# Kernel tuning notes

Measured on AMD Instinct MI355X. Metric: run time of the kernel, lower is better.

## Reference

```python
import jax, jax.numpy as jnp
import numpy as np
from jax import lax

B = 8          # batch
IMG = 224      # image size
PATCH = 16     # patch size / stride
D = 384        # embed_dim = d_model = d_inner (expand=1)
DEPTH = 24     # number of blocks
N = 16         # d_state
K = 4          # d_conv
R = 24         # dt_rank = ceil(D/16)
H = D * 4 * 2 // 3   # SwiGLU hidden = 1024
L = (IMG // PATCH) ** 2  # 196 tokens


def setup_inputs() -> dict:
    ks = iter(jax.random.split(jax.random.key(0), 40))
    def rn(shape, s=0.02):
        return jax.random.normal(next(ks), shape, jnp.float32) * s
    inp = {}
    inp["x"] = jax.random.normal(next(ks), (B, 3, IMG, IMG), jnp.float32)
    inp["patch_w"] = rn((D, 3, PATCH, PATCH))
    inp["patch_b"] = jnp.zeros((D,), jnp.float32)
    inp["norm1_w"] = jnp.ones((DEPTH, D), jnp.float32)
    inp["norm1_b"] = jnp.zeros((DEPTH, D), jnp.float32)
    inp["in_proj_w"] = rn((DEPTH, 2 * D, D))
    inp["conv_w"] = rn((DEPTH, D, K), 0.1)
    inp["conv_b"] = jnp.zeros((DEPTH, D), jnp.float32)
    inp["x_proj_w"] = rn((DEPTH, R + 2 * N, D))
    inp["dt_proj_w"] = rn((DEPTH, D, R), 0.1)
    inp["dt_proj_b"] = rn((DEPTH, D), 0.1)
    # S4D-real init: A = -exp(A_log), A_log = log(1..N)
    inp["A_log"] = jnp.tile(jnp.log(jnp.arange(1, N + 1, dtype=jnp.float32))[None, None, :], (DEPTH, D, 1))
    inp["D_skip"] = jnp.ones((DEPTH, D), jnp.float32)
    inp["out_proj_w"] = rn((DEPTH, D, D))
    inp["norm2_w"] = jnp.ones((DEPTH, D), jnp.float32)
    inp["norm2_b"] = jnp.zeros((DEPTH, D), jnp.float32)
    inp["w1_w"] = rn((DEPTH, H, D)); inp["w1_b"] = jnp.zeros((DEPTH, H), jnp.float32)
    inp["w2_w"] = rn((DEPTH, H, D)); inp["w2_b"] = jnp.zeros((DEPTH, H), jnp.float32)
    inp["w3_w"] = rn((DEPTH, D, H)); inp["w3_b"] = jnp.zeros((DEPTH, D), jnp.float32)
    inp["normf_w"] = jnp.ones((D,), jnp.float32)
    inp["normf_b"] = jnp.zeros((D,), jnp.float32)
    return inp


def _ln(x, w, b, eps=1e-5):
    m = x.mean(-1, keepdims=True)
    v = jnp.mean((x - m) ** 2, axis=-1, keepdims=True)
    return (x - m) / jnp.sqrt(v + eps) * w + b


def _mamba(x, in_w, cw, cb, xp_w, dtw, dtb, a_log, d_skip, ow):
    # x: [B, L, D]; Mamba with expand=1, bimamba 'none'
    bsz, seq, _ = x.shape
    xz = jnp.einsum('bld,ed->ble', x, in_w)        # [B, L, 2D]
    xc, z = jnp.split(xz, 2, axis=-1)
    # causal depthwise conv1d, kernel K, padding K-1, truncated to L
    xpd = jnp.pad(xc, ((0, 0), (K - 1, 0), (0, 0)))
    xconv = sum(xpd[:, k:k + seq, :] * cw[:, k] for k in range(K)) + cb
    xa = jax.nn.silu(xconv)
    dbc = jnp.einsum('bld,ed->ble', xa, xp_w)      # [B, L, R+2N]
    dt = jax.nn.softplus(jnp.einsum('blr,dr->bld', dbc[..., :R], dtw) + dtb)  # [B, L, D]
    Bm = dbc[..., R:R + N]                         # [B, L, N]
    Cm = dbc[..., R + N:]                          # [B, L, N]
    A = -jnp.exp(a_log)                            # [D, N]

    def step(h, t):
        dt_t, B_t, C_t, x_t = t                    # [B,D],[B,N],[B,N],[B,D]
        h = h * jnp.exp(dt_t[..., None] * A) + (dt_t * x_t)[..., None] * B_t[:, None, :]
        return h, jnp.einsum('bdn,bn->bd', h, C_t)

    h0 = jnp.zeros((bsz, D, N), x.dtype)
    _, ys = lax.scan(step, h0, (dt.transpose(1, 0, 2), Bm.transpose(1, 0, 2),
                                Cm.transpose(1, 0, 2), xa.transpose(1, 0, 2)))
    y = ys.transpose(1, 0, 2) + d_skip * xa
    y = y * jax.nn.silu(z)
    return jnp.einsum('bld,ed->ble', y, ow)


def _forward(x, patch_w, patch_b, norm1_w, norm1_b, in_proj_w, conv_w, conv_b,
             x_proj_w, dt_proj_w, dt_proj_b, A_log, D_skip, out_proj_w,
             norm2_w, norm2_b, w1_w, w1_b, w2_w, w2_b, w3_w, w3_b, normf_w, normf_b):
    p = lax.conv_general_dilated(x, patch_w, (PATCH, PATCH), 'VALID',
                                 dimension_numbers=('NCHW', 'OIHW', 'NCHW'))
    p = p + patch_b[None, :, None, None]
    h = p.reshape(p.shape[0], D, -1).transpose(0, 2, 1)   # [B, L, D]
    for i in range(DEPTH):
        h = h + _mamba(_ln(h, norm1_w[i], norm1_b[i]), in_proj_w[i], conv_w[i], conv_b[i],
                       x_proj_w[i], dt_proj_w[i], dt_proj_b[i], A_log[i], D_skip[i], out_proj_w[i])
        hn = _ln(h, norm2_w[i], norm2_b[i])
        hid = jax.nn.silu(hn @ w1_w[i].T + w1_b[i]) * (hn @ w2_w[i].T + w2_b[i])
        h = h + hid @ w3_w[i].T + w3_b[i]
    return _ln(h, normf_w, normf_b)


def reference(x, patch_w, patch_b, norm1_w, norm1_b, in_proj_w, conv_w, conv_b,
              x_proj_w, dt_proj_w, dt_proj_b, A_log, D_skip, out_proj_w,
              norm2_w, norm2_b, w1_w, w1_b, w2_w, w2_b, w3_w, w3_b, normf_w, normf_b):
    return _forward(x, patch_w, patch_b, norm1_w, norm1_b, in_proj_w, conv_w, conv_b,
                    x_proj_w, dt_proj_w, dt_proj_b, A_log, D_skip, out_proj_w,
                    norm2_w, norm2_b, w1_w, w1_b, w2_w, w2_b, w3_w, w3_b, normf_w, normf_b)
```

## Files before the change

kernel.cpp:

```cpp
#include <hip/hip_runtime.h>
#include <math.h>

#define BB 8
#define LL 196
#define DD 384
#define NDEPTH 24
#define NST 16
#define RRANK 24
#define HHID 1024
#define MROWS (BB*LL)
#define NCH 28
#define CHL 7

typedef float f32x4 __attribute__((ext_vector_type(4)));
typedef short s16x8 __attribute__((ext_vector_type(8)));
typedef short s16x4 __attribute__((ext_vector_type(4)));
typedef __bf16 b16x8 __attribute__((ext_vector_type(8)));
typedef unsigned short u16;
typedef unsigned int u32;

#if defined(__has_builtin)
#  if __has_builtin(__builtin_amdgcn_global_load_lds)
#    define HAS_GLL 1
#  endif
#endif
#ifndef HAS_GLL
#  define HAS_GLL 0
#endif

__device__ __forceinline__ float sigmoidf_(float x){ return 1.f/(1.f+__expf(-x)); }

__device__ __forceinline__ u16 f2bf(float f){
    u32 u = __builtin_bit_cast(u32, f);
    u32 r = (u + 0x7fffu + ((u >> 16) & 1u)) >> 16;
    return (u16)r;
}
__device__ __forceinline__ float bf2f(u16 v){
    u32 u = ((u32)v) << 16;
    return __builtin_bit_cast(float, u);
}

__device__ __forceinline__ void gll16(const u16* g, void* lds){
#if HAS_GLL
    __builtin_amdgcn_global_load_lds(
        (const __attribute__((address_space(1))) unsigned int*)g,
        (__attribute__((address_space(3))) unsigned int*)lds, 16, 0, 0);
#endif
}

template<int N> __device__ __forceinline__ void waitbar(){
    if constexpr (N==0) asm volatile("s_waitcnt vmcnt(0) lgkmcnt(0)\ns_barrier" ::: "memory");
    else if constexpr (N==4) asm volatile("s_waitcnt vmcnt(4) lgkmcnt(0)\ns_barrier" ::: "memory");
    else if constexpr (N==8) asm volatile("s_waitcnt vmcnt(8) lgkmcnt(0)\ns_barrier" ::: "memory");
    else asm volatile("s_waitcnt vmcnt(0) lgkmcnt(0)\ns_barrier" ::: "memory");
    __builtin_amdgcn_sched_barrier(0);
}
__device__ __forceinline__ void bar_release(){
    asm volatile("s_waitcnt lgkmcnt(0)\ns_barrier" ::: "memory");
    __builtin_amdgcn_sched_barrier(0);
}

template<typename V>
__device__ __forceinline__ auto mfma_try(V a, V b, f32x4 c, int)
    -> decltype(__builtin_amdgcn_mfma_f32_16x16x32_bf16(a, b, c, 0, 0, 0))
{ return __builtin_amdgcn_mfma_f32_16x16x32_bf16(a, b, c, 0, 0, 0); }

template<typename V>
__device__ __forceinline__ f32x4 mfma_try(V a, V b, f32x4 c, long)
{
    return __builtin_amdgcn_mfma_f32_16x16x32_bf16(
        __builtin_bit_cast(b16x8, a), __builtin_bit_cast(b16x8, b), c, 0, 0, 0);
}
__device__ __forceinline__ f32x4 mfma_bf16(s16x8 a, s16x8 b, f32x4 c){ return mfma_try(a, b, c, 0); }

__global__ __launch_bounds__(64) void ln_k(const float* __restrict__ X,
    const float* __restrict__ w, const float* __restrict__ b, float* __restrict__ Y)
{
    int row = blockIdx.x;
    int lane = threadIdx.x;
    const float* x = X + (size_t)row*DD;
    float v[6]; float s=0.f, s2=0.f;
    #pragma unroll
    for (int j=0;j<6;j++){ float t = x[lane + j*64]; v[j]=t; s+=t; s2+=t*t; }
    #pragma unroll
    for (int o=32;o>=1;o>>=1){ s += __shfl_xor(s,o); s2 += __shfl_xor(s2,o); }
    float m = s*(1.f/DD);
    float var = s2*(1.f/DD) - m*m;
    float rstd = rsqrtf(var + 1e-5f);
    #pragma unroll
    for (int j=0;j<6;j++){
        int c = lane + j*64;
        Y[(size_t)row*DD + c] = (v[j]-m)*rstd*w[c] + b[c];
    }
}

__global__ void gather_k(const float* __restrict__ x, u16* __restrict__ P)
{
    int idx = blockIdx.x*blockDim.x + threadIdx.x;
    if (idx >= MROWS*768) return;
    int k = idx % 768;
    int bl = idx / 768;
    int l = bl % LL;
    int b = bl / LL;
    int c = k >> 8;
    int rem = k & 255;
    int dy = rem >> 4, dx = rem & 15;
    int py = l / 14, px = l % 14;
    P[idx] = f2bf(x[(((size_t)b*3 + c)*224 + (py*16+dy))*224 + (px*16+dx)]);
}

__device__ __forceinline__ int swz(int row, int chunk){
    return (row << 7) + ((chunk ^ (row & 7)) << 4);
}

template<int EPI, bool WB, int CFG, int PRO, int K>
__global__ __launch_bounds__(256) void mgemm_k(
    const u16* __restrict__ A, const float* __restrict__ Af,
    const float* __restrict__ lnw, const float* __restrict__ lnb,
    const void* __restrict__ W1v, const void* __restrict__ W2v,
    const float* __restrict__ bias1, const float* __restrict__ bias2,
    float* __restrict__ Cf, u16* __restrict__ Cb,
    int M, int N)
{
    constexpr int  BM   = (CFG==1)?32:16;
    constexpr int  FM   = (CFG==2)?1:2;
    constexpr int  FN   = 2;
    constexpr int  NAR  = (BM+31)/32;
    constexpr bool DUAL = (EPI==4);
    constexpr int  ABY  = BM*128;
    constexpr int  BBY  = 128*128;
    constexpr bool ASY  = WB && (HAS_GLL==1);
    constexpr int  NKT  = K >> 6;
    constexpr int  NLW  = DUAL ? 8 : 4;
    __shared__ __attribute__((aligned(16))) char sm[2*ABY + 2*BBY + (DUAL ? 2*BBY : 0)];
    char* A0 = sm;          char* A1 = sm + ABY;
    char* B0 = sm + 2*ABY;  char* B1 = B0 + BBY;
    char* C0 = B1 + BBY;    char* C1 = C0 + BBY;

    const int tid = threadIdx.x;
    const int row0 = blockIdx.y * BM;
    const int col0 = blockIdx.x << 7;
    const int w = tid >> 6, lane = tid & 63;
    const int wn  = w;
    const int lr = lane & 15, lk = lane >> 4;
    const int ar0 = tid >> 3, ac8 = tid & 7;
    const bool apart = (CFG != 2) || (tid < 128);

    const u16*   W1b = (const u16*)W1v;
    const u16*   W2b = (const u16*)W2v;
    const float* W1f = (const float*)W1v;
    const float* W2f = (const float*)W2v;

    f32x4 acc [FM][FN] = {};
    f32x4 acc2[FM][FN] = {};

    s16x8 aval[NAR];
    s16x8 bval[4], b2val[4];
    float4 bvf[8], b2vf[8];
    s16x8 lnr[(PRO==1)?NKT:1];

    if (PRO == 1 && apart){
        const float* xrow = Af + (size_t)(row0 + ar0)*DD;
        float4 va[6], vb[6];
        float s = 0.f, s2 = 0.f;
        #pragma unroll
        for (int j=0;j<6;j++){
            va[j] = *(const float4*)(xrow + j*64 + ac8*8);
            vb[j] = *(const float4*)(xrow + j*64 + ac8*8 + 4);
            s  += va[j].x+va[j].y+va[j].z+va[j].w + vb[j].x+vb[j].y+vb[j].z+vb[j].w;
            s2 += va[j].x*va[j].x+va[j].y*va[j].y+va[j].z*va[j].z+va[j].w*va[j].w
                + vb[j].x*vb[j].x+vb[j].y*vb[j].y+vb[j].z*vb[j].z+vb[j].w*vb[j].w;
        }
        #pragma unroll
        for (int o=1;o<8;o<<=1){ s += __shfl_xor(s,o); s2 += __shfl_xor(s2,o); }
        float m = s*(1.f/DD);
        float rstd = rsqrtf(s2*(1.f/DD) - m*m + 1e-5f);
        #pragma unroll
        for (int j=0;j<6;j++){
            int c0 = j*64 + ac8*8;
            float4 w0 = *(const float4*)(lnw + c0);
            float4 w1 = *(const float4*)(lnw + c0 + 4);
            float4 b0 = *(const float4*)(lnb + c0);
            float4 b1 = *(const float4*)(lnb + c0 + 4);
            s16x8 ov;
            ov[0]=(short)f2bf((va[j].x-m)*rstd*w0.x+b0.x);
            ov[1]=(short)f2bf((va[j].y-m)*rstd*w0.y+b0.y);
            ov[2]=(short)f2bf((va[j].z-m)*rstd*w0.z+b0.z);
            ov[3]=(short)f2bf((va[j].w-m)*rstd*w0.w+b0.w);
            ov[4]=(short)f2bf((vb[j].x-m)*rstd*w1.x+b1.x);
            ov[5]=(short)f2bf((vb[j].y-m)*rstd*w1.y+b1.y);
            ov[6]=(short)f2bf((vb[j].z-m)*rstd*w1.z+b1.z);
            ov[7]=(short)f2bf((vb[j].w-m)*rstd*w1.w+b1.w);
            if (j < NKT) lnr[j] = ov;
        }
    }

    auto stageAsync = [&](int kt, char* bA, char* bB, char* bC){
        const int lhi = lane >> 3, llo = lane & 7;
        const int colel = (kt << 6) + ((llo ^ lhi) << 3);
        if (PRO == 0){
            constexpr int ACH = BM/8;
            #pragma unroll
            for (int ci = w; ci < ACH; ci += 4){
                int gr = row0 + ci*8 + lhi;
                gll16(A + (size_t)gr*K + colel, bA + ci*1024);
            }
        }
        #pragma unroll
        for (int i=0;i<4;i++){
            int ci = w*4 + i;
            int gb = col0 + ci*8 + lhi;
            gll16(W1b + (size_t)gb*K + colel, bB + ci*1024);
        }
        if (DUAL){
            #pragma unroll
            for (int i=0;i<4;i++){
                int ci = w*4 + i;
                int gb = col0 + ci*8 + lhi;
                gll16(W2b + (size_t)gb*K + colel, bC + ci*1024);
            }
        }
    };

    auto loadT = [&](int kt){
        const int kb = kt << 6;
        if (PRO == 0 && apart){
            #pragma unroll
            for (int i=0;i<NAR;i++){
                int gr = row0 + i*32 + ar0;
                if (gr < M) aval[i] = *(const s16x8*)(A + (size_t)gr*K + kb + ac8*8);
                else        aval[i] = s16x8{0,0,0,0,0,0,0,0};
            }
        }
        if (WB){
            #pragma unroll
            for (int i=0;i<4;i++){
                int gb = col0 + i*32 + ar0;
                if (gb < N) bval[i] = *(const s16x8*)(W1b + (size_t)gb*K + kb + ac8*8);
                else        bval[i] = s16x8{0,0,0,0,0,0,0,0};
            }
            if (DUAL){
                #pragma unroll
                for (int i=0;i<4;i++){
                    int gb = col0 + i*32 + ar0;
                    if (gb < N) b2val[i] = *(const s16x8*)(W2b + (size_t)gb*K + kb + ac8*8);
                    else        b2val[i] = s16x8{0,0,0,0,0,0,0,0};
                }
            }
        } else {
            #pragma unroll
            for (int i=0;i<8;i++){
                int ss = i*256 + tid;
                int r = ss >> 4, q = ss & 15;
                int gb = col0 + r;
                if (gb < N) bvf[i] = *(const float4*)(W1f + (size_t)gb*K + kb + q*4);
                else        bvf[i] = float4{0,0,0,0};
            }
            if (DUAL){
                #pragma unroll
                for (int i=0;i<8;i++){
                    int ss = i*256 + tid;
                    int r = ss >> 4, q = ss & 15;
                    int gb = col0 + r;
                    if (gb < N) b2vf[i] = *(const float4*)(W2f + (size_t)gb*K + kb + q*4);
                    else        b2vf[i] = float4{0,0,0,0};
                }
            }
        }
    };
    auto writeT = [&](char* bA, char* bB, char* bC){
        if (PRO == 0 && apart){
            #pragma unroll
            for (int i=0;i<NAR;i++)
                *(s16x8*)(bA + swz(i*32 + ar0, ac8)) = aval[i];
        }
        if (WB){
            #pragma unroll
            for (int i=0;i<4;i++)
                *(s16x8*)(bB + swz(i*32 + ar0, ac8)) = bval[i];
            if (DUAL){
                #pragma unroll
                for (int i=0;i<4;i++)
                    *(s16x8*)(bC + swz(i*32 + ar0, ac8)) = b2val[i];
            }
        } else {
            #pragma unroll
            for (int i=0;i<8;i++){
                int ss = i*256 + tid;
                int r = ss >> 4, q = ss & 15;
                float4 v = bvf[i];
                s16x4 cv = { (short)f2bf(v.x), (short)f2bf(v.y), (short)f2bf(v.z), (short)f2bf(v.w) };
                int off = (r << 7) + (((q >> 1) ^ (r & 7)) << 4) + ((q & 1) << 3);
                *(s16x4*)(bB + off) = cv;
            }
            if (DUAL){
                #pragma unroll
                for (int i=0;i<8;i++){
                    int ss = i*256 + tid;
                    int r = ss >> 4, q = ss & 15;
                    float4 v = b2vf[i];
                    s16x4 cv = { (short)f2bf(v.x), (short)f2bf(v.y), (short)f2bf(v.z), (short)f2bf(v.w) };
                    int off = (r << 7) + (((q >> 1) ^ (r & 7)) << 4) + ((q & 1) << 3);
                    *(s16x4*)(bC + off) = cv;
                }
            }
        }
    };

    auto compute = [&](char* cA, char* cB, char* cC){
        #pragma unroll
        for (int ks=0; ks<2; ks++){
            s16x8 af[FM], bfr[FN];
            #pragma unroll
            for (int m=0;m<FM;m++)
                af[m] = *(const s16x8*)(cA + swz(m*16 + lr, ks*4 + lk));
            #pragma unroll
            for (int n=0;n<FN;n++)
                bfr[n] = *(const s16x8*)(cB + swz(wn*32 + n*16 + lr, ks*4 + lk));
            #pragma unroll
            for (int m=0;m<FM;m++)
                #pragma unroll
                for (int n=0;n<FN;n++)
                    acc[m][n] = mfma_bf16(af[m], bfr[n], acc[m][n]);
            if (DUAL){
                s16x8 b2r[FN];
                #pragma unroll
                for (int n=0;n<FN;n++)
                    b2r[n] = *(const s16x8*)(cC + swz(wn*32 + n*16 + lr, ks*4 + lk));
                #pragma unroll
                for (int m=0;m<FM;m++)
                    #pragma unroll
                    for (int n=0;n<FN;n++)
                        acc2[m][n] = mfma_bf16(af[m], b2r[n], acc2[m][n]);
            }
        }
    };

    if (ASY){
        stageAsync(0, A0, B0, C0);
        if (NKT > 1) stageAsync(1, A1, B1, C1);
        if (PRO == 1 && apart){
            *(s16x8*)(A0 + swz(ar0, ac8)) = lnr[0];
            if (NKT > 1) *(s16x8*)(A1 + swz(ar0, ac8)) = lnr[(1 < NKT) ? 1 : 0];
        }
        if (NKT > 1) waitbar<NLW>(); else waitbar<0>();
        #pragma unroll
        for (int kt=0; kt<NKT; kt++){
            if (kt & 1) compute(A1, B1, C1);
            else        compute(A0, B0, C0);
            if (kt+1 < NKT){
                bar_release();
                if (kt+2 < NKT){
                    char* rA = (kt&1)?A1:A0; char* rB = (kt&1)?B1:B0; char* rC = (kt&1)?C1:C0;
                    stageAsync(kt+2, rA, rB, rC);
                    if (PRO == 1 && apart)
                        *(s16x8*)(rA + swz(ar0, ac8)) = lnr[(kt+2 < NKT) ? (kt+2) : 0];
                    waitbar<NLW>();
                } else {
                    waitbar<0>();
                }
            }
        }
    } else {
        loadT(0); writeT(A0, B0, C0);
        if (PRO == 1 && apart) *(s16x8*)(A0 + swz(ar0, ac8)) = lnr[0];
        __syncthreads();
        #pragma unroll
        for (int kt=0; kt<NKT; kt++){
            const bool more = (kt+1 < NKT);
            char* nA = (kt&1)?A0:A1; char* nB = (kt&1)?B0:B1; char* nC = (kt&1)?C0:C1;
            if (more){
                loadT(kt+1);
                if (PRO == 1 && apart) *(s16x8*)(nA + swz(ar0, ac8)) = lnr[(kt+1 < NKT) ? (kt+1) : 0];
            }
            if (kt & 1) compute(A1, B1, C1);
            else        compute(A0, B0, C0);
            if (more) writeT(nA, nB, nC);
            __syncthreads();
        }
    }

    #pragma unroll
    for (int n=0;n<FN;n++){
        int gc = col0 + wn*32 + n*16 + lr;
        if (gc >= N) continue;
        float b1 = 0.f, b2 = 0.f;
        if (EPI==1||EPI==3||EPI==4) b1 = bias1[gc];
        if (EPI==4) b2 = bias2[gc];
        #pragma unroll
        for (int m=0;m<FM;m++){
            #pragma unroll
            for (int r=0;r<4;r++){
                int gr = row0 + m*16 + lk*4 + r;
                if (gr >= M) continue;
                float v = acc[m][n][r];
                if (EPI==1||EPI==3) v += b1;
                if (EPI==2||EPI==3) v += Cf[(size_t)gr*N + gc];
                if (EPI==4){
                    float v1 = v + b1;
                    float v2 = acc2[m][n][r] + b2;
                    Cb[(size_t)gr*N + gc] = f2bf(v1 * sigmoidf_(v1) * v2);
                } else if (EPI==6){
                    Cb[(size_t)gr*N + gc] = f2bf(v);
                } else {
                    Cf[(size_t)gr*N + gc] = v;
                }
            }
        }
    }
}

template<int K>
__device__ __forceinline__ int off_a(int row, int chunk){
    return row*(K*2) + ((chunk ^ (row & 7)) << 4);
}

template<bool WB>
__global__ __launch_bounds__(256) void xproj_k(
    const u16* __restrict__ xzb,
    const float* __restrict__ cw, const float* __restrict__ cb,
    const void* __restrict__ Wv,
    float* __restrict__ dbc)
{
    constexpr int K = DD, N = 56;
    constexpr int ABY = 16*K*2;
    __shared__ __attribute__((aligned(16))) char sm[ABY + 2*16384];
    char* sA = sm;
    char* B0 = sm + ABY;
    char* B1 = B0 + 16384;

    const int tid = threadIdx.x;
    const int row0 = blockIdx.x * 16;
    const int wv = tid >> 6, lane = tid & 63;
    const int lr = lane & 15, lk = lane >> 4;
    const int ar0 = tid >> 3, ac8 = tid & 7;

    const u16*   Wb = (const u16*)Wv;
    const float* Wf = (const float*)Wv;

    f32x4 acc[2] = {};
    s16x8 bval[4];
    float4 bvf[8];

    auto loadB = [&](int kt){
        const int kb = kt << 6;
        if (WB){
            #pragma unroll
            for (int i=0;i<4;i++){
                int gb = i*32 + ar0;
                if (gb < N) bval[i] = *(const s16x8*)(Wb + (size_t)gb*K + kb + ac8*8);
                else        bval[i] = s16x8{0,0,0,0,0,0,0,0};
            }
        } else {
            #pragma unroll
            for (int i=0;i<8;i++){
                int ss = i*256 + tid;
                int r = ss >> 4, q = ss & 15;
                if (r < N) bvf[i] = *(const float4*)(Wf + (size_t)r*K + kb + q*4);
                else       bvf[i] = float4{0,0,0,0};
            }
        }
    };
    auto writeB = [&](char* bB){
        if (WB){
            #pragma unroll
            for (int i=0;i<4;i++)
                *(s16x8*)(bB + swz(i*32 + ar0, ac8)) = bval[i];
        } else {
            #pragma unroll
            for (int i=0;i<8;i++){
                int ss = i*256 + tid;
                int r = ss >> 4, q = ss & 15;
                float4 v = bvf[i];
                s16x4 cv = { (short)f2bf(v.x), (short)f2bf(v.y), (short)f2bf(v.z), (short)f2bf(v.w) };
                int off = (r << 7) + (((q >> 1) ^ (r & 7)) << 4) + ((q & 1) << 3);
                *(s16x4*)(bB + off) = cv;
            }
        }
    };

    loadB(0);

    #pragma unroll
    for (int r=0;r<4;r++){
        int rl = wv*4 + r, gr = row0 + rl;
        if (lane < 48){
            int l = gr % LL, bb = gr / LL;
            int d0 = lane*8;
            float a[8];
            #pragma unroll
            for (int j=0;j<8;j++) a[j] = cb[d0+j];
            #pragma unroll
            for (int t=0;t<4;t++){
                int ls = l - 3 + t;
                if (ls >= 0){
                    s16x8 xv = *(const s16x8*)(xzb + (size_t)(bb*LL+ls)*768 + d0);
                    #pragma unroll
                    for (int j=0;j<8;j++)
                        a[j] = fmaf(bf2f((u16)xv[j]), cw[(d0+j)*4+t], a[j]);
                }
            }
            s16x8 ov;
            #pragma unroll
            for (int j=0;j<8;j++)
                ov[j] = (short)f2bf(a[j]*sigmoidf_(a[j]));
            *(s16x8*)(sA + off_a<K>(rl, lane)) = ov;
        }
    }

    writeB(B0);
    __syncthreads();

    constexpr int nkt = K >> 6;
    #pragma unroll
    for (int kt=0; kt<nkt; kt++){
        const bool more = (kt+1 < nkt);
        if (more) loadB(kt+1);
        char* cB = (kt & 1) ? B1 : B0;
        #pragma unroll
        for (int ks=0; ks<2; ks++){
            s16x8 af = *(const s16x8*)(sA + off_a<K>(lr, kt*8 + ks*4 + lk));
            #pragma unroll
            for (int n=0;n<2;n++){
                s16x8 bfr = *(const s16x8*)(cB + swz(wv*32 + n*16 + lr, ks*4 + lk));
                acc[n] = mfma_bf16(af, bfr, acc[n]);
            }
        }
        if (more) writeB((kt & 1) ? B0 : B1);
        __syncthreads();
    }

    #pragma unroll
    for (int n=0;n<2;n++){
        int gc = wv*32 + n*16 + lr;
        if (gc >= N) continue;
        #pragma unroll
        for (int r=0;r<4;r++){
            int gr = row0 + lk*4 + r;
            dbc[(size_t)gr*N + gc] = acc[n][r];
        }
    }
}

__global__ void cvtw_k(const float* __restrict__ s, u16* __restrict__ d, int n)
{
    int i = blockIdx.x*blockDim.x + threadIdx.x;
    int idx = i*4;
    if (idx + 4 <= n){
        float4 v = *(const float4*)(s + idx);
        s16x4 cv = { (short)f2bf(v.x), (short)f2bf(v.y), (short)f2bf(v.z), (short)f2bf(v.w) };
        *(s16x4*)(d + idx) = cv;
    } else {
        for (int j=idx;j<n;j++) d[j] = f2bf(s[j]);
    }
}

__global__ __launch_bounds__(384) void scanA_k(
    const float* __restrict__ dbc, const u16* __restrict__ xzb,
    const float* __restrict__ cw, const float* __restrict__ cb,
    const float* __restrict__ dtw, const float* __restrict__ dtb,
    const float* __restrict__ a_log,
    float* __restrict__ Pout, float* __restrict__ Sout,
    float2* __restrict__ dtxv)
{
    int b = blockIdx.x / NCH;
    int c = blockIdx.x % NCH;
    int d = threadIdx.x;
    __shared__ float Ds[CHL][56];
    for (int t = threadIdx.x; t < CHL*56; t += 384){
        int j = t/56, q = t%56;
        Ds[j][q] = dbc[(size_t)(b*LL + c*CHL + j)*56 + q];
    }
    __syncthreads();
    float cwr[4];
    #pragma unroll
    for (int k=0;k<4;k++) cwr[k] = cw[d*4+k];
    float cbv = cb[d];
    float dtwr[RRANK];
    #pragma unroll
    for (int r=0;r<RRANK;r++) dtwr[r] = dtw[d*RRANK + r];
    float dtbv = dtb[d];
    float Aa[NST];
    #pragma unroll
    for (int n=0;n<NST;n++) Aa[n] = -__expf(a_log[d*NST+n]);
    int l0 = c*CHL;
    float p3=0.f, p2=0.f, p1=0.f;
    if (l0 >= 3) p3 = bf2f(xzb[(size_t)(b*LL+l0-3)*768 + d]);
    if (l0 >= 2) p2 = bf2f(xzb[(size_t)(b*LL+l0-2)*768 + d]);
    if (l0 >= 1) p1 = bf2f(xzb[(size_t)(b*LL+l0-1)*768 + d]);
    float hst[NST], P[NST];
    #pragma unroll
    for (int n=0;n<NST;n++){ hst[n]=0.f; P[n]=1.f; }
    #pragma unroll
    for (int j=0;j<CHL;j++){
        int row = b*LL + l0 + j;
        float cur = bf2f(xzb[(size_t)row*768 + d]);
        float a = cbv;
        a = fmaf(p3, cwr[0], a); a = fmaf(p2, cwr[1], a);
        a = fmaf(p1, cwr[2], a); a = fmaf(cur, cwr[3], a);
        p3 = p2; p2 = p1; p1 = cur;
        float xv = a * sigmoidf_(a);
        float t = dtbv;
        #pragma unroll
        for (int r=0;r<RRANK;r++) t = fmaf(dtwr[r], Ds[j][r], t);
        float dtv = (t > 20.f) ? t : log1pf(__expf(t));
        dtxv[(size_t)row*DD + d] = float2{dtv, xv};
        float du = dtv*xv;
        #pragma unroll
        for (int n=0;n<NST;n++){
            float e = __expf(dtv*Aa[n]);
            hst[n] = fmaf(hst[n], e, du*Ds[j][24+n]);
            P[n] *= e;
        }
    }
    size_t base = ((size_t)(b*NCH + c)*DD + d)*NST;
    #pragma unroll
    for (int n=0;n<NST;n++){ Pout[base+n]=P[n]; Sout[base+n]=hst[n]; }
}

__global__ __launch_bounds__(384) void scanC_k(
    const float* __restrict__ dbc, const float2* __restrict__ dtxv,
    const u16* __restrict__ xzb, const float* __restrict__ a_log,
    const float* __restrict__ Pin, const float* __restrict__ Sin,
    const float* __restrict__ dskip,
    u16* __restrict__ yg)
{
    int b = blockIdx.x / NCH;
    int c = blockIdx.x % NCH;
    int d = threadIdx.x;
    __shared__ float Ds[CHL][56];
    for (int t = threadIdx.x; t < CHL*56; t += 384){
        int j = t/56, q = t%56;
        Ds[j][q] = dbc[(size_t)(b*LL + c*CHL + j)*56 + q];
    }
    __syncthreads();
    float hst[NST];
    #pragma unroll
    for (int n=0;n<NST;n++) hst[n]=0.f;
    for (int cc=0; cc<c; cc++){
        size_t base = ((size_t)(b*NCH + cc)*DD + d)*NST;
        #pragma unroll
        for (int n=0;n<NST;n++)
            hst[n] = fmaf(Pin[base+n], hst[n], Sin[base+n]);
    }
    float Aa[NST];
    #pragma unroll
    for (int n=0;n<NST;n++) Aa[n] = -__expf(a_log[d*NST+n]);
    float dsk = dskip[d];
    int l0 = c*CHL;
    #pragma unroll
    for (int j=0;j<CHL;j++){
        int row = b*LL + l0 + j;
        float2 dx = dtxv[(size_t)row*DD + d];
        float dtv = dx.x, xv = dx.y;
        float du = dtv*xv;
        float y = 0.f;
        #pragma unroll
        for (int n=0;n<NST;n++){
            float e = __expf(dtv*Aa[n]);
            hst[n] = fmaf(hst[n], e, du*Ds[j][24+n]);
            y = fmaf(hst[n], Ds[j][40+n], y);
        }
        float zv = bf2f(xzb[(size_t)row*768 + 384 + d]);
        float g = zv * sigmoidf_(zv);
        yg[(size_t)row*DD + d] = f2bf((y + dsk*xv)*g);
    }
}

template<int EPI, int CFG, int PRO, int K>
static void mg(bool wb, dim3 g, hipStream_t s,
               const void* A, const float* Af, const float* lnw, const float* lnb,
               const void* Wb, const void* Wf, const void* W2b, const void* W2f,
               const float* b1, const float* b2, float* Cf, u16* Cb,
               int M, int N)
{
    if (wb) mgemm_k<EPI,true ,CFG,PRO,K><<<g,256,0,s>>>((const u16*)A, Af, lnw, lnb, Wb, W2b, b1, b2, Cf, Cb, M, N);
    else    mgemm_k<EPI,false,CFG,PRO,K><<<g,256,0,s>>>((const u16*)A, Af, lnw, lnb, Wf, W2f, b1, b2, Cf, Cb, M, N);
}

extern "C" void kernel_launch(void* const* d_in, const int* in_sizes, int n_in,
                              void* d_out, int out_size, void* d_ws, size_t ws_size,
                              hipStream_t stream)
{
    const float* x         = (const float*)d_in[0];
    const float* patch_w   = (const float*)d_in[1];
    const float* patch_b   = (const float*)d_in[2];
    const float* norm1_w   = (const float*)d_in[3];
    const float* norm1_b   = (const float*)d_in[4];
    const float* in_proj_w = (const float*)d_in[5];
    const float* conv_w    = (const float*)d_in[6];
    const float* conv_b    = (const float*)d_in[7];
    const float* x_proj_w  = (const float*)d_in[8];
    const float* dt_w      = (const float*)d_in[9];
    const float* dt_b      = (const float*)d_in[10];
    const float* A_log     = (const float*)d_in[11];
    const float* D_skip    = (const float*)d_in[12];
    const float* out_w     = (const float*)d_in[13];
    const float* norm2_w   = (const float*)d_in[14];
    const float* norm2_b   = (const float*)d_in[15];
    const float* w1_w      = (const float*)d_in[16];
    const float* w1_b      = (const float*)d_in[17];
    const float* w2_w      = (const float*)d_in[18];
    const float* w2_b      = (const float*)d_in[19];
    const float* w3_w      = (const float*)d_in[20];
    const float* w3_b      = (const float*)d_in[21];
    const float* normf_w   = (const float*)d_in[22];
    const float* normf_b   = (const float*)d_in[23];

    char* wsb = (char*)d_ws;
    size_t o = 0;
    auto take = [&](size_t bytes) -> char* {
        char* p = wsb + o;
        o += (bytes + 255) & ~(size_t)255;
        return p;
    };

    float* h    = (float*)take((size_t)602112*4);
    float* dbc  = (float*)take((size_t)87808*4);
    float* Pb   = (float*)take((size_t)BB*NCH*DD*NST*4);
    float* Sb   = (float*)take((size_t)BB*NCH*DD*NST*4);
    float2* dtxv= (float2*)take((size_t)MROWS*DD*8);
    u16*  xzb   = (u16*)take((size_t)1204224*2);
    u16*  yg    = (u16*)take((size_t)602112*2);
    u16*  hid   = (u16*)take((size_t)1605632*2);
    u16*  patches = hid;

    const size_t NPW = 294912, NIN = 7077888, NOUT = 3538944,
                 NW1 = 9437184, NW2 = 9437184, NW3 = 9437184, NXP = 516096;
    u16* wcP = (u16*)take(NPW*2);
    u16* wcI = (u16*)take(NIN*2);
    u16* wcO = (u16*)take(NOUT*2);
    u16* wc1 = (u16*)take(NW1*2);
    u16* wc2 = (u16*)take(NW2*2);
    u16* wc3 = (u16*)take(NW3*2);
    u16* wcX = (u16*)take(NXP*2);
    bool wb = (ws_size >= o);

    if (wb){
        cvtw_k<<<(int)((NPW/4+255)/256), 256, 0, stream>>>(patch_w, wcP, (int)NPW);
        cvtw_k<<<(int)((NIN/4+255)/256), 256, 0, stream>>>(in_proj_w, wcI, (int)NIN);
        cvtw_k<<<(int)((NOUT/4+255)/256),256, 0, stream>>>(out_w, wcO, (int)NOUT);
        cvtw_k<<<(int)((NW1/4+255)/256), 256, 0, stream>>>(w1_w, wc1, (int)NW1);
        cvtw_k<<<(int)((NW2/4+255)/256), 256, 0, stream>>>(w2_w, wc2, (int)NW2);
        cvtw_k<<<(int)((NW3/4+255)/256), 256, 0, stream>>>(w3_w, wc3, (int)NW3);
        cvtw_k<<<(int)((NXP/4+255)/256), 256, 0, stream>>>(x_proj_w, wcX, (int)NXP);
    }

    const int GY32 = MROWS/32;
    const int GY16 = MROWS/16;

    gather_k<<<(MROWS*768+255)/256, 256, 0, stream>>>(x, patches);
    mg<1,2,0,768>(wb, dim3(3,GY16), stream, patches, nullptr, nullptr, nullptr,
              wcP, patch_w, nullptr, nullptr, patch_b, nullptr, h, nullptr, MROWS, DD);

    for (int i=0;i<NDEPTH;i++){
        mg<6,1,1,384>(wb, dim3(6,GY32), stream, nullptr, h, norm1_w + i*DD, norm1_b + i*DD,
                  wcI + (size_t)i*768*DD, in_proj_w + (size_t)i*768*DD, nullptr, nullptr,
                  nullptr, nullptr, nullptr, xzb, MROWS, 768);
        if (wb) xproj_k<true ><<<GY16, 256, 0, stream>>>(xzb, conv_w + i*DD*4, conv_b + i*DD,
                                                         wcX + (size_t)i*56*DD, dbc);
        else    xproj_k<false><<<GY16, 256, 0, stream>>>(xzb, conv_w + i*DD*4, conv_b + i*DD,
                                                         x_proj_w + (size_t)i*56*DD, dbc);
        scanA_k<<<BB*NCH, 384, 0, stream>>>(dbc, xzb, conv_w + i*DD*4, conv_b + i*DD,
                                            dt_w + (size_t)i*DD*RRANK, dt_b + i*DD,
                                            A_log + (size_t)i*DD*NST, Pb, Sb, dtxv);
        scanC_k<<<BB*NCH, 384, 0, stream>>>(dbc, dtxv, xzb, A_log + (size_t)i*DD*NST,
                                            Pb, Sb, D_skip + i*DD, yg);
        mg<2,2,0,384>(wb, dim3(3,GY16), stream, yg, nullptr, nullptr, nullptr,
                  wcO + (size_t)i*DD*DD, out_w + (size_t)i*DD*DD, nullptr, nullptr,
                  nullptr, nullptr, h, nullptr, MROWS, DD);
        mg<4,1,1,384>(wb, dim3(8,GY32), stream, nullptr, h, norm2_w + i*DD, norm2_b + i*DD,
                  wc1 + (size_t)i*HHID*DD, w1_w + (size_t)i*HHID*DD,
                  wc2 + (size_t)i*HHID*DD, w2_w + (size_t)i*HHID*DD,
                  w1_b + i*HHID, w2_b + i*HHID, nullptr, hid, MROWS, HHID);
        mg<3,2,0,1024>(wb, dim3(3,GY16), stream, hid, nullptr, nullptr, nullptr,
                  wc3 + (size_t)i*DD*HHID, w3_w + (size_t)i*DD*HHID, nullptr, nullptr,
                  w3_b + i*DD, nullptr, h, nullptr, MROWS, DD);
    }

    ln_k<<<MROWS, 64, 0, stream>>>(h, normf_w, normf_b, (float*)d_out);
}
```

Measured before the change: 2.408 ms.

## Fuse chunked scan passes into one kernel with per-batch spin barrier

Merges the two selective-scan kernels into a single launch. Each block keeps its dt and x values in registers and waits on a per-batch atomic counter until every chunk of that batch has written its carry (P, S), then runs the second pass directly. This removes one launch per layer and the dtxv round trip through global memory. In exchange it depends on all 224 blocks being co-resident to avoid deadlock, and adds spin-wait and fence overhead.

```diff
diff --git a/kernel.cpp b/kernel.cpp
--- a/kernel.cpp
+++ b/kernel.cpp
@@ -555,13 +555,18 @@
     }
 }
 
-__global__ __launch_bounds__(384) void scanA_k(
+__global__ void zflag_k(u32* __restrict__ f){
+    if (threadIdx.x < NDEPTH*BB) f[threadIdx.x] = 0u;
+}
+
+__global__ __launch_bounds__(384) void scanAC_k(
     const float* __restrict__ dbc, const u16* __restrict__ xzb,
     const float* __restrict__ cw, const float* __restrict__ cb,
     const float* __restrict__ dtw, const float* __restrict__ dtb,
     const float* __restrict__ a_log,
     float* __restrict__ Pout, float* __restrict__ Sout,
-    float2* __restrict__ dtxv)
+    const float* __restrict__ dskip, u16* __restrict__ yg,
+    u32* __restrict__ flag)
 {
     int b = blockIdx.x / NCH;
     int c = blockIdx.x % NCH;
@@ -572,6 +577,7 @@
         Ds[j][q] = dbc[(size_t)(b*LL + c*CHL + j)*56 + q];
     }
     __syncthreads();
+
     float cwr[4];
     #pragma unroll
     for (int k=0;k<4;k++) cwr[k] = cw[d*4+k];
@@ -583,87 +589,79 @@
     float Aa[NST];
     #pragma unroll
     for (int n=0;n<NST;n++) Aa[n] = -__expf(a_log[d*NST+n]);
+
     int l0 = c*CHL;
     float p3=0.f, p2=0.f, p1=0.f;
     if (l0 >= 3) p3 = bf2f(xzb[(size_t)(b*LL+l0-3)*768 + d]);
     if (l0 >= 2) p2 = bf2f(xzb[(size_t)(b*LL+l0-2)*768 + d]);
     if (l0 >= 1) p1 = bf2f(xzb[(size_t)(b*LL+l0-1)*768 + d]);
-    float hst[NST], P[NST];
-    #pragma unroll
-    for (int n=0;n<NST;n++){ hst[n]=0.f; P[n]=1.f; }
-    #pragma unroll
-    for (int j=0;j<CHL;j++){
-        int row = b*LL + l0 + j;
-        float cur = bf2f(xzb[(size_t)row*768 + d]);
-        float a = cbv;
-        a = fmaf(p3, cwr[0], a); a = fmaf(p2, cwr[1], a);
-        a = fmaf(p1, cwr[2], a); a = fmaf(cur, cwr[3], a);
-        p3 = p2; p2 = p1; p1 = cur;
-        float xv = a * sigmoidf_(a);
-        float t = dtbv;
-        #pragma unroll
-        for (int r=0;r<RRANK;r++) t = fmaf(dtwr[r], Ds[j][r], t);
-        float dtv = (t > 20.f) ? t : log1pf(__expf(t));
-        dtxv[(size_t)row*DD + d] = float2{dtv, xv};
-        float du = dtv*xv;
-        #pragma unroll
-        for (int n=0;n<NST;n++){
-            float e = __expf(dtv*Aa[n]);
-            hst[n] = fmaf(hst[n], e, du*Ds[j][24+n]);
-            P[n] *= e;
-        }
-    }
-    size_t base = ((size_t)(b*NCH + c)*DD + d)*NST;
-    #pragma unroll
-    for (int n=0;n<NST;n++){ Pout[base+n]=P[n]; Sout[base+n]=hst[n]; }
-}
-
-__global__ __launch_bounds__(384) void scanC_k(
-    const float* __restrict__ dbc, const float2* __restrict__ dtxv,
-    const u16* __restrict__ xzb, const float* __restrict__ a_log,
-    const float* __restrict__ Pin, const float* __restrict__ Sin,
-    const float* __restrict__ dskip,
-    u16* __restrict__ yg)
-{
-    int b = blockIdx.x / NCH;
-    int c = blockIdx.x % NCH;
-    int d = threadIdx.x;
-    __shared__ float Ds[CHL][56];
-    for (int t = threadIdx.x; t < CHL*56; t += 384){
-        int j = t/56, q = t%56;
-        Ds[j][q] = dbc[(size_t)(b*LL + c*CHL + j)*56 + q];
-    }
+
+    float dtv[CHL], xv[CHL];
+    {
+        float hst[NST], P[NST];
+        #pragma unroll
+        for (int n=0;n<NST;n++){ hst[n]=0.f; P[n]=1.f; }
+        #pragma unroll
+        for (int j=0;j<CHL;j++){
+            int row = b*LL + l0 + j;
+            float cur = bf2f(xzb[(size_t)row*768 + d]);
+            float a = cbv;
+            a = fmaf(p3, cwr[0], a); a = fmaf(p2, cwr[1], a);
+            a = fmaf(p1, cwr[2], a); a = fmaf(cur, cwr[3], a);
+            p3 = p2; p2 = p1; p1 = cur;
+            xv[j] = a * sigmoidf_(a);
+            float t = dtbv;
+            #pragma unroll
+            for (int r=0;r<RRANK;r++) t = fmaf(dtwr[r], Ds[j][r], t);
+            dtv[j] = (t > 20.f) ? t : log1pf(__expf(t));
+            float du = dtv[j]*xv[j];
+            #pragma unroll
+            for (int n=0;n<NST;n++){
+                float e = __expf(dtv[j]*Aa[n]);
+                hst[n] = fmaf(hst[n], e, du*Ds[j][24+n]);
+                P[n] *= e;
+            }
+        }
+        size_t base = ((size_t)(b*NCH + c)*DD + d)*NST;
+        #pragma unroll
+        for (int n=0;n<NST;n++){ Pout[base+n]=P[n]; Sout[base+n]=hst[n]; }
+    }
+
+    __threadfence();
     __syncthreads();
-    float hst[NST];
-    #pragma unroll
-    for (int n=0;n<NST;n++) hst[n]=0.f;
-    for (int cc=0; cc<c; cc++){
-        size_t base = ((size_t)(b*NCH + cc)*DD + d)*NST;
-        #pragma unroll
-        for (int n=0;n<NST;n++)
-            hst[n] = fmaf(Pin[base+n], hst[n], Sin[base+n]);
-    }
-    float Aa[NST];
-    #pragma unroll
-    for (int n=0;n<NST;n++) Aa[n] = -__expf(a_log[d*NST+n]);
-    float dsk = dskip[d];
-    int l0 = c*CHL;
-    #pragma unroll
-    for (int j=0;j<CHL;j++){
-        int row = b*LL + l0 + j;
-        float2 dx = dtxv[(size_t)row*DD + d];
-        float dtv = dx.x, xv = dx.y;
-        float du = dtv*xv;
-        float y = 0.f;
-        #pragma unroll
-        for (int n=0;n<NST;n++){
-            float e = __expf(dtv*Aa[n]);
-            hst[n] = fmaf(hst[n], e, du*Ds[j][24+n]);
-            y = fmaf(hst[n], Ds[j][40+n], y);
-        }
-        float zv = bf2f(xzb[(size_t)row*768 + 384 + d]);
-        float g = zv * sigmoidf_(zv);
-        yg[(size_t)row*DD + d] = f2bf((y + dsk*xv)*g);
+    if (threadIdx.x == 0){
+        atomicAdd(&flag[b], 1u);
+        while (atomicAdd(&flag[b], 0u) < (u32)NCH) { }
+    }
+    __syncthreads();
+    __threadfence();
+
+    {
+        float hst[NST];
+        #pragma unroll
+        for (int n=0;n<NST;n++) hst[n]=0.f;
+        for (int cc=0; cc<c; cc++){
+            size_t base = ((size_t)(b*NCH + cc)*DD + d)*NST;
+            #pragma unroll
+            for (int n=0;n<NST;n++)
+                hst[n] = fmaf(Pout[base+n], hst[n], Sout[base+n]);
+        }
+        float dsk = dskip[d];
+        #pragma unroll
+        for (int j=0;j<CHL;j++){
+            int row = b*LL + l0 + j;
+            float du = dtv[j]*xv[j];
+            float y = 0.f;
+            #pragma unroll
+            for (int n=0;n<NST;n++){
+                float e = __expf(dtv[j]*Aa[n]);
+                hst[n] = fmaf(hst[n], e, du*Ds[j][24+n]);
+                y = fmaf(hst[n], Ds[j][40+n], y);
+            }
+            float zv = bf2f(xzb[(size_t)row*768 + 384 + d]);
+            float g = zv * sigmoidf_(zv);
+            yg[(size_t)row*DD + d] = f2bf((y + dsk*xv[j])*g);
+        }
     }
 }
 
@@ -719,7 +717,7 @@
     float* dbc  = (float*)take((size_t)87808*4);
     float* Pb   = (float*)take((size_t)BB*NCH*DD*NST*4);
     float* Sb   = (float*)take((size_t)BB*NCH*DD*NST*4);
-    float2* dtxv= (float2*)take((size_t)MROWS*DD*8);
+    u32*  flags = (u32*)take((size_t)NDEPTH*BB*4);
     u16*  xzb   = (u16*)take((size_t)1204224*2);
     u16*  yg    = (u16*)take((size_t)602112*2);
     u16*  hid   = (u16*)take((size_t)1605632*2);
@@ -736,6 +734,7 @@
     u16* wcX = (u16*)take(NXP*2);
     bool wb = (ws_size >= o);
 
+    zflag_k<<<1, 256, 0, stream>>>(flags);
     if (wb){
         cvtw_k<<<(int)((NPW/4+255)/256), 256, 0, stream>>>(patch_w, wcP, (int)NPW);
         cvtw_k<<<(int)((NIN/4+255)/256), 256, 0, stream>>>(in_proj_w, wcI, (int)NIN);
@@ -761,11 +760,10 @@
                                                          wcX + (size_t)i*56*DD, dbc);
         else    xproj_k<false><<<GY16, 256, 0, stream>>>(xzb, conv_w + i*DD*4, conv_b + i*DD,
                                                          x_proj_w + (size_t)i*56*DD, dbc);
-        scanA_k<<<BB*NCH, 384, 0, stream>>>(dbc, xzb, conv_w + i*DD*4, conv_b + i*DD,
-                                            dt_w + (size_t)i*DD*RRANK, dt_b + i*DD,
-                                            A_log + (size_t)i*DD*NST, Pb, Sb, dtxv);
-        scanC_k<<<BB*NCH, 384, 0, stream>>>(dbc, dtxv, xzb, A_log + (size_t)i*DD*NST,
-                                            Pb, Sb, D_skip + i*DD, yg);
+        scanAC_k<<<BB*NCH, 384, 0, stream>>>(dbc, xzb, conv_w + i*DD*4, conv_b + i*DD,
+                                             dt_w + (size_t)i*DD*RRANK, dt_b + i*DD,
+                                             A_log + (size_t)i*DD*NST, Pb, Sb,
+                                             D_skip + i*DD, yg, flags + (size_t)i*BB);
         mg<2,2,0,384>(wb, dim3(3,GY16), stream, yg, nullptr, nullptr, nullptr,
                   wcO + (size_t)i*DD*DD, out_w + (size_t)i*DD*DD, nullptr, nullptr,
                   nullptr, nullptr, h, nullptr, MROWS, DD);
```

After: 4.236 ms. 1.76x slower.

## Prefetch GEMM residual early and async-stage x_proj weights into LDS

Applied to the files above, without the earlier changes.

In the general GEMM, residual values for the residual epilogues are loaded into registers before the main loop instead of during the epilogue, so their global-load latency overlaps the K loop. In the x_proj kernel, weight tiles are copied into LDS with async global-to-LDS loads, double-buffered two tiles ahead with counter-based waits and barriers, replacing the register load/write path. This adds register pressure for the residual values and more complex synchronisation.

```diff
diff --git a/kernel.cpp b/kernel.cpp
--- a/kernel.cpp
+++ b/kernel.cpp
@@ -127,6 +127,7 @@
     constexpr int  FN   = 2;
     constexpr int  NAR  = (BM+31)/32;
     constexpr bool DUAL = (EPI==4);
+    constexpr bool RES  = (EPI==2 || EPI==3);
     constexpr int  ABY  = BM*128;
     constexpr int  BBY  = 128*128;
     constexpr bool ASY  = WB && (HAS_GLL==1);
@@ -153,6 +154,22 @@
 
     f32x4 acc [FM][FN] = {};
     f32x4 acc2[FM][FN] = {};
+
+    float cres[FM][FN][4];
+    if (RES){
+        #pragma unroll
+        for (int n=0;n<FN;n++){
+            int gc = col0 + wn*32 + n*16 + lr;
+            #pragma unroll
+            for (int m=0;m<FM;m++){
+                #pragma unroll
+                for (int r=0;r<4;r++){
+                    int gr = row0 + m*16 + lk*4 + r;
+                    cres[m][n][r] = (gc < N && gr < M) ? Cf[(size_t)gr*N + gc] : 0.f;
+                }
+            }
+        }
+    }
 
     s16x8 aval[NAR];
     s16x8 bval[4], b2val[4];
@@ -395,7 +412,7 @@
                 if (gr >= M) continue;
                 float v = acc[m][n][r];
                 if (EPI==1||EPI==3) v += b1;
-                if (EPI==2||EPI==3) v += Cf[(size_t)gr*N + gc];
+                if (RES) v += cres[m][n][r];
                 if (EPI==4){
                     float v1 = v + b1;
                     float v2 = acc2[m][n][r] + b2;
@@ -424,6 +441,7 @@
 {
     constexpr int K = DD, N = 56;
     constexpr int ABY = 16*K*2;
+    constexpr bool ASY = WB && (HAS_GLL==1);
     __shared__ __attribute__((aligned(16))) char sm[ABY + 2*16384];
     char* sA = sm;
     char* B0 = sm + ABY;
@@ -441,6 +459,18 @@
     f32x4 acc[2] = {};
     s16x8 bval[4];
     float4 bvf[8];
+
+    auto stageB = [&](int kt, char* bB){
+        const int lhi = lane >> 3, llo = lane & 7;
+        const int colel = (kt << 6) + ((llo ^ lhi) << 3);
+        #pragma unroll
+        for (int i=0;i<4;i++){
+            int ci = wv*4 + i;
+            int gb = ci*8 + lhi;
+            int gbc = (gb < N) ? gb : (N-1);
+            gll16(Wb + (size_t)gbc*K + colel, bB + ci*1024);
+        }
+    };
 
     auto loadB = [&](int kt){
         const int kb = kt << 6;
@@ -479,7 +509,8 @@
         }
     };
 
-    loadB(0);
+    if (ASY){ stageB(0, B0); stageB(1, B1); }
+    else loadB(0);
 
     #pragma unroll
     for (int r=0;r<4;r++){
@@ -508,26 +539,51 @@
         }
     }
 
-    writeB(B0);
-    __syncthreads();
-
     constexpr int nkt = K >> 6;
-    #pragma unroll
-    for (int kt=0; kt<nkt; kt++){
-        const bool more = (kt+1 < nkt);
-        if (more) loadB(kt+1);
-        char* cB = (kt & 1) ? B1 : B0;
-        #pragma unroll
-        for (int ks=0; ks<2; ks++){
-            s16x8 af = *(const s16x8*)(sA + off_a<K>(lr, kt*8 + ks*4 + lk));
-            #pragma unroll
-            for (int n=0;n<2;n++){
-                s16x8 bfr = *(const s16x8*)(cB + swz(wv*32 + n*16 + lr, ks*4 + lk));
-                acc[n] = mfma_bf16(af, bfr, acc[n]);
-            }
-        }
-        if (more) writeB((kt & 1) ? B0 : B1);
+    if (ASY){
+        waitbar<4>();
+        #pragma unroll
+        for (int kt=0; kt<nkt; kt++){
+            char* cB = (kt & 1) ? B1 : B0;
+            #pragma unroll
+            for (int ks=0; ks<2; ks++){
+                s16x8 af = *(const s16x8*)(sA + off_a<K>(lr, kt*8 + ks*4 + lk));
+                #pragma unroll
+                for (int n=0;n<2;n++){
+                    s16x8 bfr = *(const s16x8*)(cB + swz(wv*32 + n*16 + lr, ks*4 + lk));
+                    acc[n] = mfma_bf16(af, bfr, acc[n]);
+                }
+            }
+            if (kt+1 < nkt){
+                bar_release();
+                if (kt+2 < nkt){
+                    stageB(kt+2, (kt & 1) ? B1 : B0);
+                    waitbar<4>();
+                } else {
+                    waitbar<0>();
+                }
+            }
+        }
+    } else {
+        writeB(B0);
         __syncthreads();
+        #pragma unroll
+        for (int kt=0; kt<nkt; kt++){
+            const bool more = (kt+1 < nkt);
+            if (more) loadB(kt+1);
+            char* cB = (kt & 1) ? B1 : B0;
+            #pragma unroll
+            for (int ks=0; ks<2; ks++){
+                s16x8 af = *(const s16x8*)(sA + off_a<K>(lr, kt*8 + ks*4 + lk));
+                #pragma unroll
+                for (int n=0;n<2;n++){
+                    s16x8 bfr = *(const s16x8*)(cB + swz(wv*32 + n*16 + lr, ks*4 + lk));
+                    acc[n] = mfma_bf16(af, bfr, acc[n]);
+                }
+            }
+            if (more) writeB((kt & 1) ? B0 : B1);
+            __syncthreads();
+        }
     }
 
     #pragma unroll
```

New measurement: 2.371 ms. Within noise of the previous version (-1.5%).

## Fuse x_proj into scanA kernel and prefetch residual in GEMM epilogue

Applied to the files above, without the earlier changes.

Removes the separate xproj_k MFMA kernel. scanA_k now computes the conv+SiLU activations into shared memory and evaluates the 56-wide x_proj dot products in fp32 scalar FMA from the original weights, writing dbc for scanC. This saves one launch per layer and the bf16 conversion of x_proj weights, but each of the 224 blocks now rereads the whole x_proj weight matrix and does serial scalar FMAs. Separately, residual-add GEMM epilogues load the Cf residual into registers at kernel start so that load overlaps the main loop, at the cost of extra registers.

```diff
diff --git a/kernel.cpp b/kernel.cpp
--- a/kernel.cpp
+++ b/kernel.cpp
@@ -127,6 +127,7 @@
     constexpr int  FN   = 2;
     constexpr int  NAR  = (BM+31)/32;
     constexpr bool DUAL = (EPI==4);
+    constexpr bool RES  = (EPI==2 || EPI==3);
     constexpr int  ABY  = BM*128;
     constexpr int  BBY  = 128*128;
     constexpr bool ASY  = WB && (HAS_GLL==1);
@@ -153,6 +154,22 @@
 
     f32x4 acc [FM][FN] = {};
     f32x4 acc2[FM][FN] = {};
+
+    float cres[FM][FN][4];
+    if (RES){
+        #pragma unroll
+        for (int n=0;n<FN;n++){
+            int gc = col0 + wn*32 + n*16 + lr;
+            #pragma unroll
+            for (int m=0;m<FM;m++){
+                #pragma unroll
+                for (int r=0;r<4;r++){
+                    int gr = row0 + m*16 + lk*4 + r;
+                    cres[m][n][r] = (gc < N && gr < M) ? Cf[(size_t)gr*N + gc] : 0.f;
+                }
+            }
+        }
+    }
 
     s16x8 aval[NAR];
     s16x8 bval[4], b2val[4];
@@ -395,7 +412,7 @@
                 if (gr >= M) continue;
                 float v = acc[m][n][r];
                 if (EPI==1||EPI==3) v += b1;
-                if (EPI==2||EPI==3) v += Cf[(size_t)gr*N + gc];
+                if (RES) v += cres[m][n][r];
                 if (EPI==4){
                     float v1 = v + b1;
                     float v2 = acc2[m][n][r] + b2;
@@ -410,138 +427,6 @@
     }
 }
 
-template<int K>
-__device__ __forceinline__ int off_a(int row, int chunk){
-    return row*(K*2) + ((chunk ^ (row & 7)) << 4);
-}
-
-template<bool WB>
-__global__ __launch_bounds__(256) void xproj_k(
-    const u16* __restrict__ xzb,
-    const float* __restrict__ cw, const float* __restrict__ cb,
-    const void* __restrict__ Wv,
-    float* __restrict__ dbc)
-{
-    constexpr int K = DD, N = 56;
-    constexpr int ABY = 16*K*2;
-    __shared__ __attribute__((aligned(16))) char sm[ABY + 2*16384];
-    char* sA = sm;
-    char* B0 = sm + ABY;
-    char* B1 = B0 + 16384;
-
-    const int tid = threadIdx.x;
-    const int row0 = blockIdx.x * 16;
-    const int wv = tid >> 6, lane = tid & 63;
-    const int lr = lane & 15, lk = lane >> 4;
-    const int ar0 = tid >> 3, ac8 = tid & 7;
-
-    const u16*   Wb = (const u16*)Wv;
-    const float* Wf = (const float*)Wv;
-
-    f32x4 acc[2] = {};
-    s16x8 bval[4];
-    float4 bvf[8];
-
-    auto loadB = [&](int kt){
-        const int kb = kt << 6;
-        if (WB){
-            #pragma unroll
-            for (int i=0;i<4;i++){
-                int gb = i*32 + ar0;
-                if (gb < N) bval[i] = *(const s16x8*)(Wb + (size_t)gb*K + kb + ac8*8);
-                else        bval[i] = s16x8{0,0,0,0,0,0,0,0};
-            }
-        } else {
-            #pragma unroll
-            for (int i=0;i<8;i++){
-                int ss = i*256 + tid;
-                int r = ss >> 4, q = ss & 15;
-                if (r < N) bvf[i] = *(const float4*)(Wf + (size_t)r*K + kb + q*4);
-                else       bvf[i] = float4{0,0,0,0};
-            }
-        }
-    };
-    auto writeB = [&](char* bB){
-        if (WB){
-            #pragma unroll
-            for (int i=0;i<4;i++)
-                *(s16x8*)(bB + swz(i*32 + ar0, ac8)) = bval[i];
-        } else {
-            #pragma unroll
-            for (int i=0;i<8;i++){
-                int ss = i*256 + tid;
-                int r = ss >> 4, q = ss & 15;
-                float4 v = bvf[i];
-                s16x4 cv = { (short)f2bf(v.x), (short)f2bf(v.y), (short)f2bf(v.z), (short)f2bf(v.w) };
-                int off = (r << 7) + (((q >> 1) ^ (r & 7)) << 4) + ((q & 1) << 3);
-                *(s16x4*)(bB + off) = cv;
-            }
-        }
-    };
-
-    loadB(0);
-
-    #pragma unroll
-    for (int r=0;r<4;r++){
-        int rl = wv*4 + r, gr = row0 + rl;
-        if (lane < 48){
-            int l = gr % LL, bb = gr / LL;
-            int d0 = lane*8;
-            float a[8];
-            #pragma unroll
-            for (int j=0;j<8;j++) a[j] = cb[d0+j];
-            #pragma unroll
-            for (int t=0;t<4;t++){
-                int ls = l - 3 + t;
-                if (ls >= 0){
-                    s16x8 xv = *(const s16x8*)(xzb + (size_t)(bb*LL+ls)*768 + d0);
-                    #pragma unroll
-                    for (int j=0;j<8;j++)
-                        a[j] = fmaf(bf2f((u16)xv[j]), cw[(d0+j)*4+t], a[j]);
-                }
-            }
-            s16x8 ov;
-            #pragma unroll
-            for (int j=0;j<8;j++)
-                ov[j] = (short)f2bf(a[j]*sigmoidf_(a[j]));
-            *(s16x8*)(sA + off_a<K>(rl, lane)) = ov;
-        }
-    }
-
-    writeB(B0);
-    __syncthreads();
-
-    constexpr int nkt = K >> 6;
-    #pragma unroll
-    for (int kt=0; kt<nkt; kt++){
-        const bool more = (kt+1 < nkt);
-        if (more) loadB(kt+1);
-        char* cB = (kt & 1) ? B1 : B0;
-        #pragma unroll
-        for (int ks=0; ks<2; ks++){
-            s16x8 af = *(const s16x8*)(sA + off_a<K>(lr, kt*8 + ks*4 + lk));
-            #pragma unroll
-            for (int n=0;n<2;n++){
-                s16x8 bfr = *(const s16x8*)(cB + swz(wv*32 + n*16 + lr, ks*4 + lk));
-                acc[n] = mfma_bf16(af, bfr, acc[n]);
-            }
-        }
-        if (more) writeB((kt & 1) ? B0 : B1);
-        __syncthreads();
-    }
-
-    #pragma unroll
-    for (int n=0;n<2;n++){
-        int gc = wv*32 + n*16 + lr;
-        if (gc >= N) continue;
-        #pragma unroll
-        for (int r=0;r<4;r++){
-            int gr = row0 + lk*4 + r;
-            dbc[(size_t)gr*N + gc] = acc[n][r];
-        }
-    }
-}
-
 __global__ void cvtw_k(const float* __restrict__ s, u16* __restrict__ d, int n)
 {
     int i = blockIdx.x*blockDim.x + threadIdx.x;
@@ -556,41 +441,29 @@
 }
 
 __global__ __launch_bounds__(384) void scanA_k(
-    const float* __restrict__ dbc, const u16* __restrict__ xzb,
+    const float* __restrict__ Wx, const u16* __restrict__ xzb,
     const float* __restrict__ cw, const float* __restrict__ cb,
     const float* __restrict__ dtw, const float* __restrict__ dtb,
     const float* __restrict__ a_log,
     float* __restrict__ Pout, float* __restrict__ Sout,
-    float2* __restrict__ dtxv)
-{
+    float2* __restrict__ dtxv, float* __restrict__ dbc)
+{
+    __shared__ float xaS[CHL][DD+4];
+    __shared__ float Ds[CHL][56];
     int b = blockIdx.x / NCH;
     int c = blockIdx.x % NCH;
     int d = threadIdx.x;
-    __shared__ float Ds[CHL][56];
-    for (int t = threadIdx.x; t < CHL*56; t += 384){
-        int j = t/56, q = t%56;
-        Ds[j][q] = dbc[(size_t)(b*LL + c*CHL + j)*56 + q];
-    }
-    __syncthreads();
+
     float cwr[4];
     #pragma unroll
     for (int k=0;k<4;k++) cwr[k] = cw[d*4+k];
     float cbv = cb[d];
-    float dtwr[RRANK];
-    #pragma unroll
-    for (int r=0;r<RRANK;r++) dtwr[r] = dtw[d*RRANK + r];
-    float dtbv = dtb[d];
-    float Aa[NST];
-    #pragma unroll
-    for (int n=0;n<NST;n++) Aa[n] = -__expf(a_log[d*NST+n]);
     int l0 = c*CHL;
     float p3=0.f, p2=0.f, p1=0.f;
     if (l0 >= 3) p3 = bf2f(xzb[(size_t)(b*LL+l0-3)*768 + d]);
     if (l0 >= 2) p2 = bf2f(xzb[(size_t)(b*LL+l0-2)*768 + d]);
     if (l0 >= 1) p1 = bf2f(xzb[(size_t)(b*LL+l0-1)*768 + d]);
-    float hst[NST], P[NST];
-    #pragma unroll
-    for (int n=0;n<NST;n++){ hst[n]=0.f; P[n]=1.f; }
+    float xv[CHL];
     #pragma unroll
     for (int j=0;j<CHL;j++){
         int row = b*LL + l0 + j;
@@ -599,13 +472,47 @@
         a = fmaf(p3, cwr[0], a); a = fmaf(p2, cwr[1], a);
         a = fmaf(p1, cwr[2], a); a = fmaf(cur, cwr[3], a);
         p3 = p2; p2 = p1; p1 = cur;
-        float xv = a * sigmoidf_(a);
+        xv[j] = a * sigmoidf_(a);
+        xaS[j][d] = xv[j];
+    }
+    __syncthreads();
+
+    for (int t = d; t < CHL*56; t += 384){
+        int q = t / CHL, j = t - q*CHL;
+        const float* Wr = Wx + (size_t)q*DD;
+        float accd = 0.f;
+        #pragma unroll 8
+        for (int dd=0; dd<DD; dd+=4){
+            float4 wv = *(const float4*)(Wr + dd);
+            accd = fmaf(xaS[j][dd],   wv.x, accd);
+            accd = fmaf(xaS[j][dd+1], wv.y, accd);
+            accd = fmaf(xaS[j][dd+2], wv.z, accd);
+            accd = fmaf(xaS[j][dd+3], wv.w, accd);
+        }
+        Ds[j][q] = accd;
+        dbc[(size_t)(b*LL + l0 + j)*56 + q] = accd;
+    }
+    __syncthreads();
+
+    float dtwr[RRANK];
+    #pragma unroll
+    for (int r=0;r<RRANK;r++) dtwr[r] = dtw[d*RRANK + r];
+    float dtbv = dtb[d];
+    float Aa[NST];
+    #pragma unroll
+    for (int n=0;n<NST;n++) Aa[n] = -__expf(a_log[d*NST+n]);
+    float hst[NST], P[NST];
+    #pragma unroll
+    for (int n=0;n<NST;n++){ hst[n]=0.f; P[n]=1.f; }
+    #pragma unroll
+    for (int j=0;j<CHL;j++){
+        int row = b*LL + l0 + j;
         float t = dtbv;
         #pragma unroll
         for (int r=0;r<RRANK;r++) t = fmaf(dtwr[r], Ds[j][r], t);
         float dtv = (t > 20.f) ? t : log1pf(__expf(t));
-        dtxv[(size_t)row*DD + d] = float2{dtv, xv};
-        float du = dtv*xv;
+        dtxv[(size_t)row*DD + d] = float2{dtv, xv[j]};
+        float du = dtv*xv[j];
         #pragma unroll
         for (int n=0;n<NST;n++){
             float e = __expf(dtv*Aa[n]);
@@ -726,14 +633,13 @@
     u16*  patches = hid;
 
     const size_t NPW = 294912, NIN = 7077888, NOUT = 3538944,
-                 NW1 = 9437184, NW2 = 9437184, NW3 = 9437184, NXP = 516096;
+                 NW1 = 9437184, NW2 = 9437184, NW3 = 9437184;
     u16* wcP = (u16*)take(NPW*2);
     u16* wcI = (u16*)take(NIN*2);
     u16* wcO = (u16*)take(NOUT*2);
     u16* wc1 = (u16*)take(NW1*2);
     u16* wc2 = (u16*)take(NW2*2);
     u16* wc3 = (u16*)take(NW3*2);
-    u16* wcX = (u16*)take(NXP*2);
     bool wb = (ws_size >= o);
 
     if (wb){
@@ -743,7 +649,6 @@
         cvtw_k<<<(int)((NW1/4+255)/256), 256, 0, stream>>>(w1_w, wc1, (int)NW1);
         cvtw_k<<<(int)((NW2/4+255)/256), 256, 0, stream>>>(w2_w, wc2, (int)NW2);
         cvtw_k<<<(int)((NW3/4+255)/256), 256, 0, stream>>>(w3_w, wc3, (int)NW3);
-        cvtw_k<<<(int)((NXP/4+255)/256), 256, 0, stream>>>(x_proj_w, wcX, (int)NXP);
     }
 
     const int GY32 = MROWS/32;
@@ -757,13 +662,10 @@
         mg<6,1,1,384>(wb, dim3(6,GY32), stream, nullptr, h, norm1_w + i*DD, norm1_b + i*DD,
                   wcI + (size_t)i*768*DD, in_proj_w + (size_t)i*768*DD, nullptr, nullptr,
                   nullptr, nullptr, nullptr, xzb, MROWS, 768);
-        if (wb) xproj_k<true ><<<GY16, 256, 0, stream>>>(xzb, conv_w + i*DD*4, conv_b + i*DD,
-                                                         wcX + (size_t)i*56*DD, dbc);
-        else    xproj_k<false><<<GY16, 256, 0, stream>>>(xzb, conv_w + i*DD*4, conv_b + i*DD,
-                                                         x_proj_w + (size_t)i*56*DD, dbc);
-        scanA_k<<<BB*NCH, 384, 0, stream>>>(dbc, xzb, conv_w + i*DD*4, conv_b + i*DD,
+        scanA_k<<<BB*NCH, 384, 0, stream>>>(x_proj_w + (size_t)i*56*DD, xzb,
+                                            conv_w + i*DD*4, conv_b + i*DD,
                                             dt_w + (size_t)i*DD*RRANK, dt_b + i*DD,
-                                            A_log + (size_t)i*DD*NST, Pb, Sb, dtxv);
+                                            A_log + (size_t)i*DD*NST, Pb, Sb, dtxv, dbc);
         scanC_k<<<BB*NCH, 384, 0, stream>>>(dbc, dtxv, xzb, A_log + (size_t)i*DD*NST,
                                             Pb, Sb, D_skip + i*DD, yg);
         mg<2,2,0,384>(wb, dim3(3,GY16), stream, yg, nullptr, nullptr, nullptr,
```

Result: faster. 2.216 ms (-8.0%).
